# Kernel tuning notes

Hardware: AMD Instinct MI355X
Metric: run time of the kernel (lower is better)

The kernel has to match this reference:

```python
import jax, jax.numpy as jnp
import numpy as np

N, K, F, H, C = 16384, 16, 3, 64, 10


def setup_inputs() -> dict:
    key = jax.random.key(0)
    ks = jax.random.split(key, 6)
    pos = jax.random.normal(ks[0], (N, F), jnp.float32)
    batch = jnp.zeros((N,), jnp.int32)  # single graph
    W1 = jax.random.normal(ks[1], (2 * F, H), jnp.float32) * 0.1
    b1 = jnp.zeros((H,), jnp.float32)
    W2 = jax.random.normal(ks[2], (2 * H, H), jnp.float32) * 0.1
    b2 = jnp.zeros((H,), jnp.float32)
    Wc = jax.random.normal(ks[3], (H, C), jnp.float32) * 0.1
    bc = jnp.zeros((C,), jnp.float32)
    return {"pos": pos, "batch": batch, "W1": W1, "b1": b1,
            "W2": W2, "b2": b2, "Wc": Wc, "bc": bc}


def knn_graph(pos, k):
    # brute-force knn with self-loops (loop=True): self has distance 0
    sq = jnp.sum(pos * pos, axis=1)
    d = sq[:, None] + sq[None, :] - 2.0 * (pos @ pos.T)  # [N, N]
    _, idx = jax.lax.top_k(-d, k)  # [N, k] nearest neighbor indices (incl. self)
    return idx


def edge_conv(x, idx, W, b):
    # message for edge j->i: Linear(concat(x_i, x_j - x_i)); aggregate by max over neighbors
    n, k = idx.shape
    xi = x[:, None, :]               # [N, 1, F]
    xj = x[idx]                      # [N, k, F]
    msg = jnp.concatenate([jnp.broadcast_to(xi, (n, k, x.shape[1])), xj - xi], axis=-1)
    m = msg @ W + b                  # [N, k, H]
    return jnp.max(m, axis=1)        # [N, H]


def reference(pos, batch, W1, b1, W2, b2, Wc, bc):
    idx = knn_graph(pos, K)
    h = jax.nn.relu(edge_conv(pos, idx, W1, b1))
    h = jax.nn.relu(edge_conv(h, idx, W2, b2))
    g = jax.ops.segment_max(h, batch, num_segments=1)  # global max pool -> [1, H]
    return g @ Wc + bc
```

## Files before the change

kernel.cpp:

```cpp
#include <hip/hip_runtime.h>

#define NPTS 16384
#define KNN 16
#define HID 64
#define NCLS 10

#define WPB 4
#define QPB 8
#define CPW (NPTS / WPB)
#define SCAP 128

__device__ __forceinline__ float distm2(float qx, float qy, float qz, float4 c) {
    return fmaf(qx, c.x, fmaf(qy, c.y, fmaf(qz, c.z, c.w)));
}

__device__ __forceinline__ unsigned long long dkey(float v, int j) {
    unsigned u = __float_as_uint(v);
    u = (u & 0x80000000u) ? ~u : (u | 0x80000000u);
    return ((unsigned long long)u << 32) | (unsigned)j;
}

__device__ __forceinline__ unsigned long long shfl_xor_u64(unsigned long long x, int m) {
    unsigned hi = (unsigned)__shfl_xor((int)(x >> 32), m, 64);
    unsigned lo = (unsigned)__shfl_xor((int)(x & 0xffffffffu), m, 64);
    return ((unsigned long long)hi << 32) | lo;
}

__device__ __forceinline__ void wave_top16_16(unsigned long long (&key)[16], int lane,
                                              int q, int* __restrict__ idx) {
    int outj = 0x7fffffff;
    for (int r = 0; r < 16; ++r) {
        unsigned long long gm = key[0];
#pragma unroll
        for (int s = 1; s < 16; ++s) gm = key[s] < gm ? key[s] : gm;
#pragma unroll
        for (int st = 1; st < 64; st <<= 1) {
            unsigned long long o = shfl_xor_u64(gm, st);
            gm = o < gm ? o : gm;
        }
        if (lane == r) outj = (int)(gm & 0xffffffffu);
#pragma unroll
        for (int s = 0; s < 16; ++s)
            if (key[s] == gm) key[s] = ~0ull;
    }
    if (lane < 16) idx[q * KNN + lane] = outj;
}

__global__ void prep_kernel(const float* __restrict__ pos, float4* __restrict__ pos4,
                            float4* __restrict__ pm2) {
    int i = blockIdx.x * 256 + threadIdx.x;
    if (i < NPTS) {
        float x = pos[3 * i], y = pos[3 * i + 1], z = pos[3 * i + 2];
        float sq = fmaf(x, x, fmaf(y, y, z * z));
        pos4[i] = make_float4(x, y, z, sq);
        pm2[i] = make_float4(-2.f * x, -2.f * y, -2.f * z, sq);
    }
}

__global__ __launch_bounds__(256) void knn_kernel(const float4* __restrict__ pos4,
                                                  const float4* __restrict__ pm2,
                                                  int* __restrict__ idx) {
    __shared__ unsigned long long keys[QPB][SCAP];
    __shared__ int knt[QPB];
    __shared__ float smin[QPB][WPB][16];
    int tid = threadIdx.x;
    int lane = tid & 63;
    int w = tid >> 6;
    int qb = blockIdx.x * QPB;
    float qx[QPB], qy[QPB], qz[QPB];
#pragma unroll
    for (int i = 0; i < QPB; ++i) {
        float4 t = pos4[qb + i];
        qx[i] = t.x; qy[i] = t.y; qz[i] = t.z;
    }
    int base = w * CPW;

    float mn[QPB];
#pragma unroll
    for (int i = 0; i < QPB; ++i) mn[i] = INFINITY;
    {
        float4 c0 = pm2[base + lane];
        float4 c1 = pm2[base + 64 + lane];
        for (int cb = base; cb < base + CPW; cb += 128) {
            float4 n0 = pm2[cb + 128 + lane];
            float4 n1 = pm2[cb + 192 + lane];
#pragma unroll
            for (int i = 0; i < QPB; ++i) mn[i] = fminf(mn[i], distm2(qx[i], qy[i], qz[i], c0));
#pragma unroll
            for (int i = 0; i < QPB; ++i) mn[i] = fminf(mn[i], distm2(qx[i], qy[i], qz[i], c1));
            c0 = n0; c1 = n1;
        }
    }
#pragma unroll
    for (int i = 0; i < QPB; ++i) {
        float m = mn[i];
        m = fminf(m, __shfl_xor(m, 16, 64));
        m = fminf(m, __shfl_xor(m, 32, 64));
        if (lane < 16) smin[i][w][lane] = m;
    }
    if (tid < QPB) knt[tid] = 0;
    __syncthreads();

    float tq[QPB];
#pragma unroll
    for (int i = 0; i < QPB; ++i) {
        int s = lane & 15;
        float m = fminf(fminf(smin[i][0][s], smin[i][1][s]),
                        fminf(smin[i][2][s], smin[i][3][s]));
        m = fmaxf(m, __shfl_xor(m, 1, 64));
        m = fmaxf(m, __shfl_xor(m, 2, 64));
        m = fmaxf(m, __shfl_xor(m, 4, 64));
        m = fmaxf(m, __shfl_xor(m, 8, 64));
        tq[i] = m;
    }

    {
        float4 c0 = pm2[base + lane];
        float4 c1 = pm2[base + 64 + lane];
        for (int cb = base; cb < base + CPW; cb += 128) {
            float4 n0 = pm2[cb + 128 + lane];
            float4 n1 = pm2[cb + 192 + lane];
            int j0 = cb + lane, j1 = cb + 64 + lane;
#pragma unroll
            for (int i = 0; i < QPB; ++i) {
                float v = distm2(qx[i], qy[i], qz[i], c0);
                if (v <= tq[i]) { int s = atomicAdd(&knt[i], 1); if (s < SCAP) keys[i][s] = dkey(v, j0); }
            }
#pragma unroll
            for (int i = 0; i < QPB; ++i) {
                float v = distm2(qx[i], qy[i], qz[i], c1);
                if (v <= tq[i]) { int s = atomicAdd(&knt[i], 1); if (s < SCAP) keys[i][s] = dkey(v, j1); }
            }
            c0 = n0; c1 = n1;
        }
    }
    __syncthreads();

#pragma unroll
    for (int e = 0; e < 2; ++e) {
        int qi = w * 2 + e;
        int q = qb + qi;
        int ntot = knt[qi];
        if (ntot <= SCAP) {
            unsigned long long k0 = (lane < ntot) ? keys[qi][lane] : ~0ull;
            unsigned long long k1 = (lane + 64 < ntot) ? keys[qi][lane + 64] : ~0ull;
            int r0 = 0, r1 = 0;
            for (int t = 0; t < ntot; ++t) {
                unsigned long long k = keys[qi][t];
                r0 += (int)(k < k0);
                r1 += (int)(k < k1);
            }
            if (lane < ntot && r0 < KNN) idx[q * KNN + r0] = (int)(k0 & 0xffffffffu);
            if (lane + 64 < ntot && r1 < KNN) idx[q * KNN + r1] = (int)(k1 & 0xffffffffu);
        } else {
            float tqq = tq[qi];
            unsigned long long key[16];
#pragma unroll
            for (int u = 0; u < 16; ++u) key[u] = ~0ull;
            for (int j = lane; j < NPTS; j += 64) {
                float v = distm2(qx[qi], qy[qi], qz[qi], pm2[j]);
                unsigned long long k = dkey(v, j);
                if (v <= tqq && k < key[15]) {
#pragma unroll
                    for (int s = 0; s < 16; ++s) {
                        unsigned long long a = k < key[s] ? k : key[s];
                        unsigned long long b = k < key[s] ? key[s] : k;
                        key[s] = a;
                        k = b;
                    }
                }
            }
            wave_top16_16(key, lane, q, idx);
        }
    }
}

__global__ __launch_bounds__(256) void ec1_kernel(const float4* __restrict__ pos4,
                                                  const int* __restrict__ idx,
                                                  const float* __restrict__ W1,
                                                  const float* __restrict__ b1,
                                                  float* __restrict__ h1) {
    int t = threadIdx.x & 63;
    int p = blockIdx.x * 4 + (threadIdx.x >> 6);
    float4 xi = pos4[p];
    float w0 = W1[0 * HID + t], w1 = W1[1 * HID + t], w2 = W1[2 * HID + t];
    float v0 = W1[3 * HID + t], v1 = W1[4 * HID + t], v2 = W1[5 * HID + t];
    float C = b1[t] + xi.x * (w0 - v0) + xi.y * (w1 - v1) + xi.z * (w2 - v2);
    float m = -INFINITY;
#pragma unroll
    for (int k = 0; k < KNN; ++k) {
        int j = idx[p * KNN + k];
        float4 xj = pos4[j];
        float y = fmaf(xj.x, v0, fmaf(xj.y, v1, xj.z * v2));
        m = fmaxf(m, y);
    }
    h1[p * HID + t] = fmaxf(C + m, 0.f);
}

__global__ __launch_bounds__(256) void ec2_pre_kernel(const float* __restrict__ h1,
                                                      const float* __restrict__ W2,
                                                      const float* __restrict__ b2,
                                                      float* __restrict__ C2,
                                                      float* __restrict__ Y2) {
    int t = threadIdx.x & 63;
    int r = threadIdx.x >> 6;
    int pb = blockIdx.x * 16 + r * 4;
    float aa[4] = {0.f, 0.f, 0.f, 0.f};
    float ab[4] = {0.f, 0.f, 0.f, 0.f};
#pragma unroll 8
    for (int f = 0; f < 64; ++f) {
        float wa = W2[f * HID + t];
        float wb = W2[(64 + f) * HID + t];
#pragma unroll
        for (int i = 0; i < 4; ++i) {
            float h = h1[(pb + i) * HID + f];
            aa[i] = fmaf(h, wa, aa[i]);
            ab[i] = fmaf(h, wb, ab[i]);
        }
    }
    float bt = b2[t];
#pragma unroll
    for (int i = 0; i < 4; ++i) {
        C2[(pb + i) * HID + t] = bt + aa[i] - ab[i];
        Y2[(pb + i) * HID + t] = ab[i];
    }
}

__global__ __launch_bounds__(256) void ec2_maxpool_kernel(const float* __restrict__ C2,
                                                          const float* __restrict__ Y2,
                                                          const int* __restrict__ idx,
                                                          float* __restrict__ gpartial) {
    int t = threadIdx.x & 63;
    int lp = threadIdx.x >> 6;
    int p = blockIdx.x * 4 + lp;
    float m = -INFINITY;
#pragma unroll
    for (int k = 0; k < KNN; ++k) {
        int j = idx[p * KNN + k];
        m = fmaxf(m, Y2[j * HID + t]);
    }
    float val = fmaxf(C2[p * HID + t] + m, 0.f);
    __shared__ float red[4][64];
    red[lp][t] = val;
    __syncthreads();
    if (lp == 0) {
        float g = fmaxf(fmaxf(red[0][t], red[1][t]), fmaxf(red[2][t], red[3][t]));
        gpartial[blockIdx.x * 64 + t] = g;
    }
}

__global__ __launch_bounds__(256) void greduce2_kernel(const float* __restrict__ gpartial,
                                                       float* __restrict__ gp2) {
    __shared__ float red[4][64];
    int f = threadIdx.x & 63;
    int w = threadIdx.x >> 6;
    int r0 = blockIdx.x * 16 + w * 4;
    float m = -INFINITY;
#pragma unroll
    for (int r = 0; r < 4; ++r) m = fmaxf(m, gpartial[(r0 + r) * 64 + f]);
    red[w][f] = m;
    __syncthreads();
    if (w == 0)
        gp2[blockIdx.x * 64 + f] =
            fmaxf(fmaxf(red[0][f], red[1][f]), fmaxf(red[2][f], red[3][f]));
}

__global__ __launch_bounds__(256) void tail2_kernel(const float* __restrict__ gp2,
                                                    const float* __restrict__ Wc,
                                                    const float* __restrict__ bc,
                                                    float* __restrict__ out) {
    __shared__ float red[4][64];
    __shared__ float g[64];
    int f = threadIdx.x & 63;
    int w = threadIdx.x >> 6;
    float m = -INFINITY;
    for (int i = w; i < 256; i += 4) m = fmaxf(m, gp2[i * 64 + f]);
    red[w][f] = m;
    __syncthreads();
    if (w == 0) g[f] = fmaxf(fmaxf(red[0][f], red[1][f]), fmaxf(red[2][f], red[3][f]));
    __syncthreads();
    if (threadIdx.x < NCLS) {
        float a = bc[threadIdx.x];
#pragma unroll
        for (int h = 0; h < HID; ++h) a = fmaf(g[h], Wc[h * NCLS + threadIdx.x], a);
        out[threadIdx.x] = a;
    }
}

extern "C" void kernel_launch(void* const* d_in, const int* in_sizes, int n_in,
                              void* d_out, int out_size, void* d_ws, size_t ws_size,
                              hipStream_t stream) {
    const float* pos = (const float*)d_in[0];
    const float* W1 = (const float*)d_in[2];
    const float* b1 = (const float*)d_in[3];
    const float* W2 = (const float*)d_in[4];
    const float* b2 = (const float*)d_in[5];
    const float* Wc = (const float*)d_in[6];
    const float* bc = (const float*)d_in[7];
    float* out = (float*)d_out;

    char* ws = (char*)d_ws;
    size_t o = 0;
    auto alloc = [&](size_t bytes) { size_t r = o; o += (bytes + 255) & ~size_t(255); return r; };
    size_t fm = (size_t)NPTS * HID * 4;
    size_t o_pos4 = alloc((size_t)NPTS * 16);
    size_t o_pm2 = alloc((size_t)(NPTS + 192) * 16);
    size_t o_idx = alloc((size_t)NPTS * KNN * 4);
    size_t o_h1 = alloc(fm);
    size_t o_C2 = alloc(fm);
    size_t o_Y2 = alloc(fm);
    size_t o_gp = alloc((size_t)(NPTS / 4) * HID * 4);
    size_t o_gp2 = alloc((size_t)256 * HID * 4);

    float4* pos4 = (float4*)(ws + o_pos4);
    float4* pm2 = (float4*)(ws + o_pm2);
    int* idx = (int*)(ws + o_idx);
    float* h1 = (float*)(ws + o_h1);
    float* C2 = (float*)(ws + o_C2);
    float* Y2 = (float*)(ws + o_Y2);
    float* gp = (float*)(ws + o_gp);
    float* gp2 = (float*)(ws + o_gp2);

    hipMemsetAsync(pm2 + NPTS, 0, 192 * sizeof(float4), stream);

    prep_kernel<<<NPTS / 256, 256, 0, stream>>>(pos, pos4, pm2);
    knn_kernel<<<NPTS / QPB, 256, 0, stream>>>(pos4, pm2, idx);
    ec1_kernel<<<NPTS / 4, 256, 0, stream>>>(pos4, idx, W1, b1, h1);
    ec2_pre_kernel<<<NPTS / 16, 256, 0, stream>>>(h1, W2, b2, C2, Y2);
    ec2_maxpool_kernel<<<NPTS / 4, 256, 0, stream>>>(C2, Y2, idx, gp);
    greduce2_kernel<<<256, 256, 0, stream>>>(gp, gp2);
    tail2_kernel<<<1, 256, 0, stream>>>(gp2, Wc, bc, out);
}
```

Before: 313.2 us.

## Fuse edge-conv1 into ec2 precompute and deepen kNN candidate prefetch

```diff
diff --git a/kernel.cpp b/kernel.cpp
--- a/kernel.cpp
+++ b/kernel.cpp
@@ -79,16 +79,16 @@
 #pragma unroll
     for (int i = 0; i < QPB; ++i) mn[i] = INFINITY;
     {
-        float4 c0 = pm2[base + lane];
-        float4 c1 = pm2[base + 64 + lane];
+        float4 c0 = pm2[base + lane],       c1 = pm2[base + 64 + lane];
+        float4 d0 = pm2[base + 128 + lane], d1 = pm2[base + 192 + lane];
         for (int cb = base; cb < base + CPW; cb += 128) {
-            float4 n0 = pm2[cb + 128 + lane];
-            float4 n1 = pm2[cb + 192 + lane];
 #pragma unroll
             for (int i = 0; i < QPB; ++i) mn[i] = fminf(mn[i], distm2(qx[i], qy[i], qz[i], c0));
 #pragma unroll
             for (int i = 0; i < QPB; ++i) mn[i] = fminf(mn[i], distm2(qx[i], qy[i], qz[i], c1));
-            c0 = n0; c1 = n1;
+            c0 = d0; c1 = d1;
+            d0 = pm2[cb + 256 + lane];
+            d1 = pm2[cb + 320 + lane];
         }
     }
 #pragma unroll
@@ -115,23 +115,22 @@
     }
 
     {
-        float4 c0 = pm2[base + lane];
-        float4 c1 = pm2[base + 64 + lane];
+        float4 c0 = pm2[base + lane],       c1 = pm2[base + 64 + lane];
+        float4 d0 = pm2[base + 128 + lane], d1 = pm2[base + 192 + lane];
         for (int cb = base; cb < base + CPW; cb += 128) {
-            float4 n0 = pm2[cb + 128 + lane];
-            float4 n1 = pm2[cb + 192 + lane];
             int j0 = cb + lane, j1 = cb + 64 + lane;
 #pragma unroll
             for (int i = 0; i < QPB; ++i) {
-                float v = distm2(qx[i], qy[i], qz[i], c0);
-                if (v <= tq[i]) { int s = atomicAdd(&knt[i], 1); if (s < SCAP) keys[i][s] = dkey(v, j0); }
+                float va = distm2(qx[i], qy[i], qz[i], c0);
+                float vb = distm2(qx[i], qy[i], qz[i], c1);
+                if (fminf(va, vb) <= tq[i]) {
+                    if (va <= tq[i]) { int s = atomicAdd(&knt[i], 1); if (s < SCAP) keys[i][s] = dkey(va, j0); }
+                    if (vb <= tq[i]) { int s = atomicAdd(&knt[i], 1); if (s < SCAP) keys[i][s] = dkey(vb, j1); }
+                }
             }
-#pragma unroll
-            for (int i = 0; i < QPB; ++i) {
-                float v = distm2(qx[i], qy[i], qz[i], c1);
-                if (v <= tq[i]) { int s = atomicAdd(&knt[i], 1); if (s < SCAP) keys[i][s] = dkey(v, j1); }
-            }
-            c0 = n0; c1 = n1;
+            c0 = d0; c1 = d1;
+            d0 = pm2[cb + 256 + lane];
+            d1 = pm2[cb + 320 + lane];
         }
     }
     __syncthreads();
@@ -175,36 +174,36 @@
     }
 }
 
-__global__ __launch_bounds__(256) void ec1_kernel(const float4* __restrict__ pos4,
-                                                  const int* __restrict__ idx,
-                                                  const float* __restrict__ W1,
-                                                  const float* __restrict__ b1,
-                                                  float* __restrict__ h1) {
+__global__ __launch_bounds__(256) void ec12_kernel(const float4* __restrict__ pos4,
+                                                   const int* __restrict__ idx,
+                                                   const float* __restrict__ W1,
+                                                   const float* __restrict__ b1,
+                                                   const float* __restrict__ W2,
+                                                   const float* __restrict__ b2,
+                                                   float* __restrict__ C2,
+                                                   float* __restrict__ Y2) {
+    __shared__ float h1s[16][64];
     int t = threadIdx.x & 63;
-    int p = blockIdx.x * 4 + (threadIdx.x >> 6);
-    float4 xi = pos4[p];
+    int w = threadIdx.x >> 6;
+    int pb = blockIdx.x * 16 + w * 4;
     float w0 = W1[0 * HID + t], w1 = W1[1 * HID + t], w2 = W1[2 * HID + t];
     float v0 = W1[3 * HID + t], v1 = W1[4 * HID + t], v2 = W1[5 * HID + t];
-    float C = b1[t] + xi.x * (w0 - v0) + xi.y * (w1 - v1) + xi.z * (w2 - v2);
-    float m = -INFINITY;
-#pragma unroll
-    for (int k = 0; k < KNN; ++k) {
-        int j = idx[p * KNN + k];
-        float4 xj = pos4[j];
-        float y = fmaf(xj.x, v0, fmaf(xj.y, v1, xj.z * v2));
-        m = fmaxf(m, y);
-    }
-    h1[p * HID + t] = fmaxf(C + m, 0.f);
-}
-
-__global__ __launch_bounds__(256) void ec2_pre_kernel(const float* __restrict__ h1,
-                                                      const float* __restrict__ W2,
-                                                      const float* __restrict__ b2,
-                                                      float* __restrict__ C2,
-                                                      float* __restrict__ Y2) {
-    int t = threadIdx.x & 63;
-    int r = threadIdx.x >> 6;
-    int pb = blockIdx.x * 16 + r * 4;
+    float bt1 = b1[t];
+#pragma unroll
+    for (int i = 0; i < 4; ++i) {
+        int p = pb + i;
+        float4 xi = pos4[p];
+        float C = bt1 + xi.x * (w0 - v0) + xi.y * (w1 - v1) + xi.z * (w2 - v2);
+        float m = -INFINITY;
+#pragma unroll
+        for (int k = 0; k < KNN; ++k) {
+            int j = idx[p * KNN + k];
+            float4 xj = pos4[j];
+            m = fmaxf(m, fmaf(xj.x, v0, fmaf(xj.y, v1, xj.z * v2)));
+        }
+        h1s[w * 4 + i][t] = fmaxf(C + m, 0.f);
+    }
+    __syncthreads();
     float aa[4] = {0.f, 0.f, 0.f, 0.f};
     float ab[4] = {0.f, 0.f, 0.f, 0.f};
 #pragma unroll 8
@@ -213,7 +212,7 @@
         float wb = W2[(64 + f) * HID + t];
 #pragma unroll
         for (int i = 0; i < 4; ++i) {
-            float h = h1[(pb + i) * HID + f];
+            float h = h1s[w * 4 + i][f];
             aa[i] = fmaf(h, wa, aa[i]);
             ab[i] = fmaf(h, wb, ab[i]);
         }
@@ -304,9 +303,8 @@
     auto alloc = [&](size_t bytes) { size_t r = o; o += (bytes + 255) & ~size_t(255); return r; };
     size_t fm = (size_t)NPTS * HID * 4;
     size_t o_pos4 = alloc((size_t)NPTS * 16);
-    size_t o_pm2 = alloc((size_t)(NPTS + 192) * 16);
+    size_t o_pm2 = alloc((size_t)(NPTS + 320) * 16);
     size_t o_idx = alloc((size_t)NPTS * KNN * 4);
-    size_t o_h1 = alloc(fm);
     size_t o_C2 = alloc(fm);
     size_t o_Y2 = alloc(fm);
     size_t o_gp = alloc((size_t)(NPTS / 4) * HID * 4);
@@ -315,18 +313,16 @@
     float4* pos4 = (float4*)(ws + o_pos4);
     float4* pm2 = (float4*)(ws + o_pm2);
     int* idx = (int*)(ws + o_idx);
-    float* h1 = (float*)(ws + o_h1);
     float* C2 = (float*)(ws + o_C2);
     float* Y2 = (float*)(ws + o_Y2);
     float* gp = (float*)(ws + o_gp);
     float* gp2 = (float*)(ws + o_gp2);
 
-    hipMemsetAsync(pm2 + NPTS, 0, 192 * sizeof(float4), stream);
+    hipMemsetAsync(pm2 + NPTS, 0, 320 * sizeof(float4), stream);
 
     prep_kernel<<<NPTS / 256, 256, 0, stream>>>(pos, pos4, pm2);
     knn_kernel<<<NPTS / QPB, 256, 0, stream>>>(pos4, pm2, idx);
-    ec1_kernel<<<NPTS / 4, 256, 0, stream>>>(pos4, idx, W1, b1, h1);
-    ec2_pre_kernel<<<NPTS / 16, 256, 0, stream>>>(h1, W2, b2, C2, Y2);
+    ec12_kernel<<<NPTS / 16, 256, 0, stream>>>(pos4, idx, W1, b1, W2, b2, C2, Y2);
     ec2_maxpool_kernel<<<NPTS / 4, 256, 0, stream>>>(C2, Y2, idx, gp);
     greduce2_kernel<<<256, 256, 0, stream>>>(gp, gp2);
     tail2_kernel<<<1, 256, 0, stream>>>(gp2, Wc, bc, out);
```

Result: faster. 306.2 us (-2.2%).
